# Kernel optimization log

Hardware: AMD Instinct MI355X
Metric: run time of the kernel (lower is better)

## Reference

```python
import jax, jax.numpy as jnp
import numpy as np

HEADS = 16
NEG = -1.0e9


def setup_inputs() -> dict:
    key = jax.random.key(0)
    ks = jax.random.split(key, 9)
    B, T, E = 2, 2048, 1024
    s = 1.0 / np.sqrt(E)
    return {
        "x": jax.random.normal(ks[0], (B, T, E), dtype=jnp.float32),
        "Wq": jax.random.normal(ks[1], (E, E), dtype=jnp.float32) * s,
        "bq": jax.random.normal(ks[2], (E,), dtype=jnp.float32) * 0.01,
        "Wk": jax.random.normal(ks[3], (E, E), dtype=jnp.float32) * s,
        "bk": jax.random.normal(ks[4], (E,), dtype=jnp.float32) * 0.01,
        "Wv": jax.random.normal(ks[5], (E, E), dtype=jnp.float32) * s,
        "bv": jax.random.normal(ks[6], (E,), dtype=jnp.float32) * 0.01,
        "Wo": jax.random.normal(ks[7], (E, E), dtype=jnp.float32) * s,
        "bo": jax.random.normal(ks[8], (E,), dtype=jnp.float32) * 0.01,
    }


def reference(x, Wq, bq, Wk, bk, Wv, bv, Wo, bo):
    B, T, E = x.shape
    H = HEADS
    D = E // H
    # In the original forward (idx_t=-2, context=None): context = x, so
    # values(x), keys(context), queries(context) all read x.
    v = (x @ Wv + bv).reshape(B, T, H, D)
    k = (x @ Wk + bk).reshape(B, T, H, D)
    q = (x @ Wq + bq).reshape(B, T, H, D)
    # causal mask: 1 above diagonal, 0 on/below; broadcast over (B, H)
    mask = 1.0 - jnp.tril(jnp.ones((T, T), dtype=x.dtype))  # [T, T]
    energy = jnp.einsum("bqhd,bkhd->bhqk", q, k)
    # Faithful to source: mask*(-1e9) added BEFORE the sqrt(embed_size) scaling
    energy = energy + mask[None, None] * jnp.asarray(NEG, dtype=x.dtype)
    attn = jax.nn.softmax(energy / jnp.sqrt(jnp.asarray(E, dtype=x.dtype)), axis=-1)
    out = jnp.einsum("bhqk,bkhd->bqhd", attn, v).reshape(B, T, E)
    return out @ Wo + bo
```

## Files before the change

### kernel.cpp

```cpp
#include <hip/hip_runtime.h>
#include <hip/hip_bf16.h>
#include <stdint.h>


typedef __attribute__((ext_vector_type(8))) short short8;
typedef __attribute__((ext_vector_type(4))) short short4v;
typedef __attribute__((ext_vector_type(4))) float f32x4;

#define MFMA16(a, b, c) __builtin_amdgcn_mfma_f32_16x16x32_bf16((a), (b), (c), 0, 0, 0)

static __device__ __forceinline__ unsigned short f2bf(float f) {
    union { float f; unsigned int u; } v; v.f = f;
    unsigned int r = v.u + 0x7fffu + ((v.u >> 16) & 1u);
    return (unsigned short)(r >> 16);
}

static __device__ __forceinline__ void gld16(const unsigned short* g,
                                             unsigned short* l) {
    __builtin_amdgcn_global_load_lds(
        (const __attribute__((address_space(1))) unsigned int*)g,
        (__attribute__((address_space(3))) unsigned int*)l, 16, 0, 0);
}

__global__ __launch_bounds__(256) void k_convert_x(const float* __restrict__ x,
                                                   unsigned short* __restrict__ xb) {
    int i = blockIdx.x * 256 + threadIdx.x;
    const float4* p = (const float4*)(x + (size_t)i * 8);
    float4 a = p[0], b = p[1];
    short8 o;
    o[0] = (short)f2bf(a.x); o[1] = (short)f2bf(a.y);
    o[2] = (short)f2bf(a.z); o[3] = (short)f2bf(a.w);
    o[4] = (short)f2bf(b.x); o[5] = (short)f2bf(b.y);
    o[6] = (short)f2bf(b.z); o[7] = (short)f2bf(b.w);
    ((short8*)xb)[i] = o;
}

__global__ __launch_bounds__(256) void k_transpose_w4(
        const float* __restrict__ W0, const float* __restrict__ W1,
        const float* __restrict__ W2, const float* __restrict__ W3,
        unsigned short* __restrict__ T0, unsigned short* __restrict__ T1,
        unsigned short* __restrict__ T2, unsigned short* __restrict__ T3) {
    const float* W = (blockIdx.z == 0) ? W0 : (blockIdx.z == 1) ? W1
                     : (blockIdx.z == 2) ? W2 : W3;
    unsigned short* Wt = (blockIdx.z == 0) ? T0 : (blockIdx.z == 1) ? T1
                         : (blockIdx.z == 2) ? T2 : T3;
    __shared__ float tw[64][68];
    const int k0 = blockIdx.x * 64, n0 = blockIdx.y * 64;
    const int tid = threadIdx.x;
#pragma unroll
    for (int r = 0; r < 4; ++r) {
        int i = tid + r * 256;
        int row = i >> 4, c4 = (i & 15) * 4;
        float4 v = *(const float4*)(W + (size_t)(k0 + row) * 1024 + n0 + c4);
        *(float4*)(&tw[row][c4]) = v;
    }
    __syncthreads();
#pragma unroll
    for (int r = 0; r < 2; ++r) {
        int i = tid + r * 256;
        int nrow = i >> 3, kc = (i & 7) * 8;
        short8 o;
#pragma unroll
        for (int j = 0; j < 8; ++j) o[j] = (short)f2bf(tw[kc + j][nrow]);
        *(short8*)(Wt + (size_t)(n0 + nrow) * 1024 + k0 + kc) = o;
    }
}

template <int MODE>
__global__ __launch_bounds__(256) void k_gemm2(const unsigned short* __restrict__ A,
                                               const unsigned short* __restrict__ Bt,
                                               const float* __restrict__ bq,
                                               const float* __restrict__ bk,
                                               const float* __restrict__ bv,
                                               unsigned short* __restrict__ Qb,
                                               unsigned short* __restrict__ Kb,
                                               unsigned short* __restrict__ Vt,
                                               float* __restrict__ Co) {
    __shared__ unsigned short As[2][128 * 32];
    __shared__ unsigned short Bs[2][128 * 32];
    const int tid = threadIdx.x;
    const int w = tid >> 6, lane = tid & 63;
    const int quad = lane >> 4, l16 = lane & 15;
    const int wm = w >> 1, wn = w & 1;
    const int m0 = blockIdx.x * 128, n0 = blockIdx.y * 128;
    const int lrow = lane >> 2, lch = (lane & 3) * 8;

    const unsigned short* ga = A + (size_t)(m0 + w * 32 + lrow) * 1024 + lch;
    const unsigned short* gb = Bt + (size_t)(n0 + w * 32 + lrow) * 1024 + lch;
    const int lofs = w * 1024 + lane * 8;

    f32x4 acc[4][4];
#pragma unroll
    for (int mt = 0; mt < 4; ++mt)
#pragma unroll
        for (int nt = 0; nt < 4; ++nt) acc[mt][nt] = (f32x4){0.f, 0.f, 0.f, 0.f};

    gld16(ga, &As[0][lofs]);
    gld16(ga + 16 * 1024, &As[0][lofs + 512]);
    gld16(gb, &Bs[0][lofs]);
    gld16(gb + 16 * 1024, &Bs[0][lofs + 512]);
    __syncthreads();

    int cur = 0;
    for (int k0 = 0; k0 < 1024; k0 += 32) {
        const bool more = (k0 + 32) < 1024;
        if (more) {
            const int nxt = cur ^ 1;
            gld16(ga + k0 + 32, &As[nxt][lofs]);
            gld16(ga + 16 * 1024 + k0 + 32, &As[nxt][lofs + 512]);
            gld16(gb + k0 + 32, &Bs[nxt][lofs]);
            gld16(gb + 16 * 1024 + k0 + 32, &Bs[nxt][lofs + 512]);
        }
        short8 af[4], bf[4];
#pragma unroll
        for (int mt = 0; mt < 4; ++mt)
            af[mt] = *(const short8*)(&As[cur][(wm * 64 + mt * 16 + l16) * 32 + quad * 8]);
#pragma unroll
        for (int nt = 0; nt < 4; ++nt)
            bf[nt] = *(const short8*)(&Bs[cur][(wn * 64 + nt * 16 + l16) * 32 + quad * 8]);
#pragma unroll
        for (int mt = 0; mt < 4; ++mt)
#pragma unroll
            for (int nt = 0; nt < 4; ++nt)
                acc[mt][nt] = MFMA16(af[mt], bf[nt], acc[mt][nt]);
        if (more) {
            __syncthreads();
            cur ^= 1;
        }
    }

    if (MODE == 1) {
#pragma unroll
        for (int nt = 0; nt < 4; ++nt) {
            int col = n0 + wn * 64 + nt * 16 + l16;
            float bb = bq[col];
#pragma unroll
            for (int mt = 0; mt < 4; ++mt) {
                int row = m0 + wm * 64 + mt * 16 + quad * 4;
#pragma unroll
                for (int r = 0; r < 4; ++r)
                    Co[(size_t)(row + r) * 1024 + col] = acc[mt][nt][r] + bb;
            }
        }
    } else if (n0 < 2048) {
        unsigned short* C = (n0 < 1024) ? Qb : Kb;
        const float* bias = (n0 < 1024) ? bq : bk;
        const float sc = (n0 < 1024) ? 0.03125f : 1.0f;
        int cb = (n0 < 1024) ? n0 : (n0 - 1024);
#pragma unroll
        for (int nt = 0; nt < 4; ++nt) {
            int col = cb + wn * 64 + nt * 16 + l16;
            float bb = bias[col];
#pragma unroll
            for (int mt = 0; mt < 4; ++mt) {
                int row = m0 + wm * 64 + mt * 16 + quad * 4;
#pragma unroll
                for (int r = 0; r < 4; ++r)
                    C[(size_t)(row + r) * 1024 + col] = f2bf((acc[mt][nt][r] + bb) * sc);
            }
        }
    } else {
#pragma unroll
        for (int nt = 0; nt < 4; ++nt) {
            int vcol = (n0 - 2048) + wn * 64 + nt * 16 + l16;
            float bb = bv[vcol];
#pragma unroll
            for (int mt = 0; mt < 4; ++mt) {
                int row = m0 + wm * 64 + mt * 16 + quad * 4;
                int b = row >> 11, t = row & 2047;
                short4v o;
#pragma unroll
                for (int r = 0; r < 4; ++r) o[r] = (short)f2bf(acc[mt][nt][r] + bb);
                *(short4v*)(&Vt[((size_t)(b * 16 + (vcol >> 6)) * 64 + (vcol & 63))
                                    * 2048 + t]) = o;
            }
        }
    }
}

__global__ __launch_bounds__(256) void k_attn(const unsigned short* __restrict__ Qb,
                                              const unsigned short* __restrict__ Kb,
                                              const unsigned short* __restrict__ Vt,
                                              unsigned short* __restrict__ Ob) {
    __shared__ unsigned short Ks[64][72];
    __shared__ unsigned short Vs[64][72];
    __shared__ unsigned short Ps[4][16][72];
    const int tid = threadIdx.x;
    const int w = tid >> 6, lane = tid & 63;
    const int quad = lane >> 4, l16 = lane & 15;
    const int id = blockIdx.x;
    const int bh = (id & 7) + 8 * ((id >> 3) & 3);
    const int g = id >> 5, gk = g & 7, gb2 = g >> 3;
    const int qb = (gb2 == 0) ? 31 - gk : (gb2 == 1) ? 16 + gk
                   : (gb2 == 2) ? 15 - gk : gk;
    const int b = bh >> 4, h = bh & 15;
    const int qg = qb * 64 + w * 16 + l16;
    const f32x4 zero4 = {0.f, 0.f, 0.f, 0.f};

    const int srow = tid >> 3, sc8 = (tid & 7) * 8;
    const unsigned short* kg0 = Kb + (size_t)(b * 2048) * 1024 + h * 64 + sc8;
    const unsigned short* vg0 = Vt + (size_t)(bh * 64 + srow) * 2048 + sc8;

    short8 qf[2];
    {
        const unsigned short* qp =
            Qb + (size_t)(b * 2048 + qg) * 1024 + h * 64 + quad * 8;
        qf[0] = *(const short8*)(qp);
        qf[1] = *(const short8*)(qp + 32);
    }
    float m_ = -1e30f, l_ = 0.f;
    f32x4 o[4];
#pragma unroll
    for (int dt = 0; dt < 4; ++dt) o[dt] = zero4;

    short8 kr0, kr1, vr0, vr1;
    kr0 = *(const short8*)(kg0 + (size_t)(srow) * 1024);
    kr1 = *(const short8*)(kg0 + (size_t)(32 + srow) * 1024);
    vr0 = *(const short8*)(vg0);
    vr1 = *(const short8*)(vg0 + (size_t)32 * 2048);
    *(short8*)(&Ks[srow][sc8]) = kr0;
    *(short8*)(&Ks[32 + srow][sc8]) = kr1;
    *(short8*)(&Vs[srow][sc8]) = vr0;
    *(short8*)(&Vs[32 + srow][sc8]) = vr1;
    __syncthreads();

    for (int kt = 0; kt <= qb; ++kt) {
        const bool more = kt < qb;
        if (more) {
            const unsigned short* kg = kg0 + (size_t)((kt + 1) * 64) * 1024;
            kr0 = *(const short8*)(kg + (size_t)(srow) * 1024);
            kr1 = *(const short8*)(kg + (size_t)(32 + srow) * 1024);
            vr0 = *(const short8*)(vg0 + (kt + 1) * 64);
            vr1 = *(const short8*)(vg0 + (size_t)32 * 2048 + (kt + 1) * 64);
        }

        f32x4 s[4];
#pragma unroll
        for (int kkt = 0; kkt < 4; ++kkt) {
            short8 kf0 = *(const short8*)(&Ks[kkt * 16 + l16][quad * 8]);
            short8 kf1 = *(const short8*)(&Ks[kkt * 16 + l16][32 + quad * 8]);
            s[kkt] = MFMA16(kf0, qf[0], zero4);
            s[kkt] = MFMA16(kf1, qf[1], s[kkt]);
        }

        if (kt == qb) {
#pragma unroll
            for (int kkt = 0; kkt < 4; ++kkt) {
                int kg_ = qb * 64 + kkt * 16 + quad * 4;
#pragma unroll
                for (int r = 0; r < 4; ++r)
                    if (kg_ + r > qg) s[kkt][r] = -1e30f;
            }
        }
        float mx = -1e30f;
#pragma unroll
        for (int kkt = 0; kkt < 4; ++kkt)
#pragma unroll
            for (int r = 0; r < 4; ++r) mx = fmaxf(mx, s[kkt][r]);
        mx = fmaxf(mx, __shfl_xor(mx, 16, 64));
        mx = fmaxf(mx, __shfl_xor(mx, 32, 64));
        const float mold = m_;
        m_ = fmaxf(m_, mx);
        float sum = 0.f;
#pragma unroll
        for (int kkt = 0; kkt < 4; ++kkt)
#pragma unroll
            for (int r = 0; r < 4; ++r) {
                float p = __expf(s[kkt][r] - m_);
                s[kkt][r] = p;
                sum += p;
            }
        sum += __shfl_xor(sum, 16, 64);
        sum += __shfl_xor(sum, 32, 64);
        if (__any(m_ > mold)) {
            float al = __expf(mold - m_);
            l_ = l_ * al + sum;
#pragma unroll
            for (int dt = 0; dt < 4; ++dt)
#pragma unroll
                for (int r = 0; r < 4; ++r) o[dt][r] *= al;
        } else {
            l_ += sum;
        }

#pragma unroll
        for (int kkt = 0; kkt < 4; ++kkt) {
            short4v pk;
#pragma unroll
            for (int r = 0; r < 4; ++r) pk[r] = (short)f2bf(s[kkt][r]);
            *(short4v*)(&Ps[w][l16][kkt * 16 + quad * 4]) = pk;
        }
        __threadfence_block();

#pragma unroll
        for (int kks = 0; kks < 2; ++kks) {
            short8 pf = *(const short8*)(&Ps[w][l16][kks * 32 + quad * 8]);
#pragma unroll
            for (int dt = 0; dt < 4; ++dt) {
                short8 vf = *(const short8*)(
                    &Vs[dt * 16 + l16][kks * 32 + quad * 8]);
                o[dt] = MFMA16(vf, pf, o[dt]);
            }
        }

        if (more) {
            __syncthreads();
            *(short8*)(&Ks[srow][sc8]) = kr0;
            *(short8*)(&Ks[32 + srow][sc8]) = kr1;
            *(short8*)(&Vs[srow][sc8]) = vr0;
            *(short8*)(&Vs[32 + srow][sc8]) = vr1;
            __syncthreads();
        }
    }

    float inv = 1.0f / l_;
    unsigned short* op = Ob + (size_t)(b * 2048 + qg) * 1024 + h * 64 + quad * 4;
#pragma unroll
    for (int dt = 0; dt < 4; ++dt) {
        short4v ov;
#pragma unroll
        for (int r = 0; r < 4; ++r) ov[r] = (short)f2bf(o[dt][r] * inv);
        *(short4v*)(op + dt * 16) = ov;
    }
}

extern "C" void kernel_launch(void* const* d_in, const int* in_sizes, int n_in,
                              void* d_out, int out_size, void* d_ws, size_t ws_size,
                              hipStream_t stream) {
    const float* x  = (const float*)d_in[0];
    const float* Wq = (const float*)d_in[1];
    const float* bq = (const float*)d_in[2];
    const float* Wk = (const float*)d_in[3];
    const float* bk = (const float*)d_in[4];
    const float* Wv = (const float*)d_in[5];
    const float* bv = (const float*)d_in[6];
    const float* Wo = (const float*)d_in[7];
    const float* bo = (const float*)d_in[8];
    float* out = (float*)d_out;

    const size_t M4 = 4194304, M1 = 1048576;
    const size_t NEED = (M4 + M4 + 3 * M1 + M1) * 2;
    if (ws_size < NEED) return;
    unsigned short* ws = (unsigned short*)d_ws;
    unsigned short* xb  = ws;
    unsigned short* Ob  = ws;
    unsigned short* Vt  = ws + M4;
    unsigned short* WtQ = ws + 2 * M4;
    unsigned short* Wto = WtQ + 3 * M1;
    unsigned short* Qb  = (unsigned short*)d_out;
    unsigned short* Kb  = Qb + M4;

    k_convert_x<<<2048, 256, 0, stream>>>(x, xb);
    k_transpose_w4<<<dim3(16, 16, 4), 256, 0, stream>>>(
        Wq, Wk, Wv, Wo, WtQ, WtQ + M1, WtQ + 2 * M1, Wto);
    k_gemm2<0><<<dim3(32, 24), 256, 0, stream>>>(xb, WtQ, bq, bk, bv,
                                                 Qb, Kb, Vt, nullptr);
    k_attn<<<1024, 256, 0, stream>>>(Qb, Kb, Vt, Ob);
    k_gemm2<1><<<dim3(32, 8), 256, 0, stream>>>(Ob, Wto, bo, nullptr, nullptr,
                                                nullptr, nullptr, nullptr, out);
}
```

Before: 205.6 us.

## Shrink GEMM N-tile to 64 and drop LDS double buffering

Halves the GEMM block's N tile from 128 to 64, which doubles grid size for the QKV and output projections (768→1536 and 256→512 blocks) to give more blocks to fill the GPU. It also removes the double-buffered LDS prefetch in favour of a single buffer with load-then-sync each k-step. This cuts LDS use and registers per block, which may raise occupancy. The cost is exposed global-load latency on every k iteration and less A-tile reuse per block.

```diff
diff --git a/kernel.cpp b/kernel.cpp
--- a/kernel.cpp
+++ b/kernel.cpp
@@ -76,63 +76,50 @@
                                                unsigned short* __restrict__ Kb,
                                                unsigned short* __restrict__ Vt,
                                                float* __restrict__ Co) {
-    __shared__ unsigned short As[2][128 * 32];
-    __shared__ unsigned short Bs[2][128 * 32];
+    __shared__ unsigned short As[128 * 32];
+    __shared__ unsigned short Bs[64 * 32];
     const int tid = threadIdx.x;
     const int w = tid >> 6, lane = tid & 63;
     const int quad = lane >> 4, l16 = lane & 15;
     const int wm = w >> 1, wn = w & 1;
-    const int m0 = blockIdx.x * 128, n0 = blockIdx.y * 128;
+    const int m0 = blockIdx.x * 128, n0 = blockIdx.y * 64;
     const int lrow = lane >> 2, lch = (lane & 3) * 8;
 
     const unsigned short* ga = A + (size_t)(m0 + w * 32 + lrow) * 1024 + lch;
-    const unsigned short* gb = Bt + (size_t)(n0 + w * 32 + lrow) * 1024 + lch;
-    const int lofs = w * 1024 + lane * 8;
-
-    f32x4 acc[4][4];
+    const unsigned short* gb = Bt + (size_t)(n0 + w * 16 + (lane >> 2)) * 1024 + lch;
+    const int lofsA = w * 1024 + lane * 8;
+    const int lofsB = w * 512 + lane * 8;
+
+    f32x4 acc[4][2];
 #pragma unroll
     for (int mt = 0; mt < 4; ++mt)
 #pragma unroll
-        for (int nt = 0; nt < 4; ++nt) acc[mt][nt] = (f32x4){0.f, 0.f, 0.f, 0.f};
-
-    gld16(ga, &As[0][lofs]);
-    gld16(ga + 16 * 1024, &As[0][lofs + 512]);
-    gld16(gb, &Bs[0][lofs]);
-    gld16(gb + 16 * 1024, &Bs[0][lofs + 512]);
-    __syncthreads();
-
-    int cur = 0;
+        for (int nt = 0; nt < 2; ++nt) acc[mt][nt] = (f32x4){0.f, 0.f, 0.f, 0.f};
+
     for (int k0 = 0; k0 < 1024; k0 += 32) {
-        const bool more = (k0 + 32) < 1024;
-        if (more) {
-            const int nxt = cur ^ 1;
-            gld16(ga + k0 + 32, &As[nxt][lofs]);
-            gld16(ga + 16 * 1024 + k0 + 32, &As[nxt][lofs + 512]);
-            gld16(gb + k0 + 32, &Bs[nxt][lofs]);
-            gld16(gb + 16 * 1024 + k0 + 32, &Bs[nxt][lofs + 512]);
-        }
-        short8 af[4], bf[4];
+        __syncthreads();
+        gld16(ga + k0, &As[lofsA]);
+        gld16(ga + 16 * 1024 + k0, &As[lofsA + 512]);
+        gld16(gb + k0, &Bs[lofsB]);
+        __syncthreads();
+        short8 af[4], bf[2];
 #pragma unroll
         for (int mt = 0; mt < 4; ++mt)
-            af[mt] = *(const short8*)(&As[cur][(wm * 64 + mt * 16 + l16) * 32 + quad * 8]);
-#pragma unroll
-        for (int nt = 0; nt < 4; ++nt)
-            bf[nt] = *(const short8*)(&Bs[cur][(wn * 64 + nt * 16 + l16) * 32 + quad * 8]);
+            af[mt] = *(const short8*)(&As[(wm * 64 + mt * 16 + l16) * 32 + quad * 8]);
+#pragma unroll
+        for (int nt = 0; nt < 2; ++nt)
+            bf[nt] = *(const short8*)(&Bs[(wn * 32 + nt * 16 + l16) * 32 + quad * 8]);
 #pragma unroll
         for (int mt = 0; mt < 4; ++mt)
 #pragma unroll
-            for (int nt = 0; nt < 4; ++nt)
+            for (int nt = 0; nt < 2; ++nt)
                 acc[mt][nt] = MFMA16(af[mt], bf[nt], acc[mt][nt]);
-        if (more) {
-            __syncthreads();
-            cur ^= 1;
-        }
     }
 
     if (MODE == 1) {
 #pragma unroll
-        for (int nt = 0; nt < 4; ++nt) {
-            int col = n0 + wn * 64 + nt * 16 + l16;
+        for (int nt = 0; nt < 2; ++nt) {
+            int col = n0 + wn * 32 + nt * 16 + l16;
             float bb = bq[col];
 #pragma unroll
             for (int mt = 0; mt < 4; ++mt) {
@@ -148,8 +135,8 @@
         const float sc = (n0 < 1024) ? 0.03125f : 1.0f;
         int cb = (n0 < 1024) ? n0 : (n0 - 1024);
 #pragma unroll
-        for (int nt = 0; nt < 4; ++nt) {
-            int col = cb + wn * 64 + nt * 16 + l16;
+        for (int nt = 0; nt < 2; ++nt) {
+            int col = cb + wn * 32 + nt * 16 + l16;
             float bb = bias[col];
 #pragma unroll
             for (int mt = 0; mt < 4; ++mt) {
@@ -161,8 +148,8 @@
         }
     } else {
 #pragma unroll
-        for (int nt = 0; nt < 4; ++nt) {
-            int vcol = (n0 - 2048) + wn * 64 + nt * 16 + l16;
+        for (int nt = 0; nt < 2; ++nt) {
+            int vcol = (n0 - 2048) + wn * 32 + nt * 16 + l16;
             float bb = bv[vcol];
 #pragma unroll
             for (int mt = 0; mt < 4; ++mt) {
@@ -353,9 +340,9 @@
     k_convert_x<<<2048, 256, 0, stream>>>(x, xb);
     k_transpose_w4<<<dim3(16, 16, 4), 256, 0, stream>>>(
         Wq, Wk, Wv, Wo, WtQ, WtQ + M1, WtQ + 2 * M1, Wto);
-    k_gemm2<0><<<dim3(32, 24), 256, 0, stream>>>(xb, WtQ, bq, bk, bv,
+    k_gemm2<0><<<dim3(32, 48), 256, 0, stream>>>(xb, WtQ, bq, bk, bv,
                                                  Qb, Kb, Vt, nullptr);
     k_attn<<<1024, 256, 0, stream>>>(Qb, Kb, Vt, Ob);
-    k_gemm2<1><<<dim3(32, 8), 256, 0, stream>>>(Ob, Wto, bo, nullptr, nullptr,
-                                                nullptr, nullptr, nullptr, out);
-}
+    k_gemm2<1><<<dim3(32, 16), 256, 0, stream>>>(Ob, Wto, bo, nullptr, nullptr,
+                                                 nullptr, nullptr, nullptr, out);
+}
```

New measurement: 196.0 us. -4.7%, faster.
